# Kernel tuning notes

Measured on AMD Instinct MI355X. Metric: run time of the kernel, lower is better.

Reference implementation:

```python
import jax, jax.numpy as jnp
import numpy as np

NUM_GROUPS = 16
MINIS_PER_GROUP = 16
MINIS_PER_TOK = 4
HIDDEN = 8192
N_TOKENS = 8192


def setup_inputs() -> dict:
    key = jax.random.key(0)
    k1, k2, k3 = jax.random.split(key, 3)
    hidden_states = jax.random.normal(k1, (N_TOKENS, HIDDEN), dtype=jnp.float32)
    # nn.Linear weight: [num_groups, hidden]
    group_gate_w = jax.random.normal(k2, (NUM_GROUPS, HIDDEN), dtype=jnp.float32) * 0.02
    # mini_gates parameter: [num_groups, hidden, minis_per_group]
    mini_gates = jax.random.normal(k3, (NUM_GROUPS, HIDDEN, MINIS_PER_GROUP), dtype=jnp.float32) * 0.02
    return {"hidden_states": hidden_states, "group_gate_w": group_gate_w, "mini_gates": mini_gates}


def reference(hidden_states, group_gate_w, mini_gates):
    # Tier 1: group gate
    group_logits = hidden_states @ group_gate_w.T                      # [N, G]
    group_probs = jax.nn.softmax(group_logits.astype(jnp.float32), axis=-1)
    top_group_probs = jnp.max(group_probs, axis=-1)                    # [N]
    top_group_indices = jnp.argmax(group_probs, axis=-1)               # [N]

    # Tier 2: per-token mini-gate. Instead of gathering a huge [N, H, E]
    # tensor (as the torch code does), compute logits for ALL groups
    # ([N, G, E] is tiny) and select the chosen group's row — same math.
    all_mini_logits = jnp.einsum('nh,ghe->nge', hidden_states, mini_gates)  # [N, G, E]
    mini_logits = jnp.take_along_axis(
        all_mini_logits, top_group_indices[:, None, None], axis=1
    )[:, 0, :]                                                         # [N, E]
    mini_probs = jax.nn.softmax(mini_logits.astype(jnp.float32), axis=-1)

    topk_mini_probs, topk_mini_indices = jax.lax.top_k(mini_probs, MINIS_PER_TOK)
    final_probs = top_group_probs[:, None] * topk_mini_probs
    final_probs = final_probs / jnp.sum(final_probs, axis=-1, keepdims=True)

    global_expert_indices = top_group_indices[:, None] * MINIS_PER_GROUP + topk_mini_indices

    group_aux_loss = jnp.sum(jnp.mean(group_probs, axis=0) ** 2)
    mini_aux_loss = jnp.sum(jnp.mean(mini_probs, axis=0) ** 2)
    total_aux_loss = group_aux_loss + mini_aux_loss

    return (final_probs.astype(hidden_states.dtype), global_expert_indices, total_aux_loss)
```

## Files before the change

kernel.cpp:

```cpp
#include <hip/hip_runtime.h>
#include <math.h>

#define N_TOK 8192
#define HID   8192
#define NG    16
#define NE    16
#define KC    512
#define NCHUNK (HID / KC)
#define TPB   16

#define OFF_CNT   0u
#define OFF_GSUM  64u
#define OFF_ESUM  128u
#define OFF_NTIL  192u
#define ZERO_BYTES 256u
#define OFF_BUCK  256u
#define OFF_SCHED (OFF_BUCK + NG*N_TOK*4)
#define OFF_MGT   (OFF_SCHED + 2048*4)

__device__ __forceinline__ void glds16(const float* gp, float* lp) {
    __builtin_amdgcn_global_load_lds(
        (const __attribute__((address_space(1))) void*)gp,
        (__attribute__((address_space(3))) void*)lp, 16, 0, 0);
}

#define RS_ROUND(o, half)                                                 \
  {                                                                       \
    const bool hi_ = (lane & (o)) != 0;                                   \
    _Pragma("unroll")                                                     \
    for (int i_ = 0; i_ < (half); ++i_) {                                 \
      double s_ = hi_ ? acc64[i_] : acc64[i_ + (half)];                   \
      double r_ = __shfl_xor(s_, (o));                                    \
      acc64[i_] = (hi_ ? acc64[i_ + (half)] : acc64[i_]) + r_;            \
    }                                                                     \
  }

#define DOT8(t, w0, w1)                                                   \
    (aC[2*(t)].x*(w0).x + aC[2*(t)].y*(w0).y + aC[2*(t)].z*(w0).z +       \
     aC[2*(t)].w*(w0).w + aC[2*(t)+1].x*(w1).x + aC[2*(t)+1].y*(w1).y +   \
     aC[2*(t)+1].z*(w1).z + aC[2*(t)+1].w*(w1).w)

__global__ __launch_bounds__(256, 2) void k_group(
    const float* __restrict__ hid, const float* __restrict__ gw,
    int* __restrict__ cnt, int* __restrict__ buckets, float* __restrict__ gsum)
{
    __shared__ float Wl[2][NG * KC];
    const int tid  = threadIdx.x;
    const int lane = tid & 63;
    const int wv   = tid >> 6;
    const int t0   = blockIdx.x * TPB + wv * 4;
    const float* __restrict__ a0 = hid + (size_t)t0 * HID;

    #pragma unroll
    for (int j = 0; j < 8; ++j) {
        int m = wv * 8 + j;
        glds16(gw + (size_t)(m >> 1) * HID + (m & 1) * 256 + 4 * lane,
               &Wl[0][m * 256]);
    }
    float4 areg[8];
    #pragma unroll
    for (int t = 0; t < 4; ++t) {
        areg[2*t]   = *(const float4*)&a0[(size_t)t * HID + 4 * lane];
        areg[2*t+1] = *(const float4*)&a0[(size_t)t * HID + 256 + 4 * lane];
    }

    double acc64[64];
    #pragma unroll
    for (int i = 0; i < 64; ++i) acc64[i] = 0.0;

    for (int c = 0; c < NCHUNK; ++c) {
        __syncthreads();
        float4 aC[8];
        #pragma unroll
        for (int i = 0; i < 8; ++i) aC[i] = areg[i];
        if (c + 1 < NCHUNK) {
            const int kb = (c + 1) * KC;
            #pragma unroll
            for (int j = 0; j < 8; ++j) {
                int m = wv * 8 + j;
                glds16(gw + (size_t)(m >> 1) * HID + kb + (m & 1) * 256 + 4 * lane,
                       &Wl[(c + 1) & 1][m * 256]);
            }
            #pragma unroll
            for (int t = 0; t < 4; ++t) {
                areg[2*t]   = *(const float4*)&a0[(size_t)t * HID + kb + 4 * lane];
                areg[2*t+1] = *(const float4*)&a0[(size_t)t * HID + kb + 256 + 4 * lane];
            }
        }
        const float* Wc = &Wl[c & 1][0];
        #pragma unroll
        for (int g = 0; g < NG; ++g) {
            float4 w0 = *(const float4*)&Wc[g * KC + 4 * lane];
            float4 w1 = *(const float4*)&Wc[g * KC + 256 + 4 * lane];
            #pragma unroll
            for (int t = 0; t < 4; ++t)
                acc64[t * 16 + g] += (double)DOT8(t, w0, w1);
        }
    }

    RS_ROUND(32, 32) RS_ROUND(16, 16) RS_ROUND(8, 8)
    RS_ROUND(4, 4)   RS_ROUND(2, 2)   RS_ROUND(1, 1)
    float v = (float)acc64[0];
    float mx = v;
    #pragma unroll
    for (int o = 8; o; o >>= 1) mx = fmaxf(mx, __shfl_xor(mx, o));
    float p = expf(v - mx);
    float s = p;
    #pragma unroll
    for (int o = 8; o; o >>= 1) s += __shfl_xor(s, o);
    p /= s;
    float x = p;
    x += __shfl_xor(x, 16);
    x += __shfl_xor(x, 32);
    if (lane < 16) unsafeAtomicAdd(&gsum[lane], x);
    int gi = lane & 15; float bv = v;
    #pragma unroll
    for (int o = 8; o; o >>= 1) {
        float ov = __shfl_xor(bv, o);
        int   og = __shfl_xor(gi, o);
        if (ov > bv || (ov == bv && og < gi)) { bv = ov; gi = og; }
    }
    if ((lane & 15) == 0) {
        int t = t0 + (lane >> 4);
        int pos = atomicAdd(&cnt[gi], 1);
        buckets[gi * N_TOK + pos] = t;
    }
}

__global__ __launch_bounds__(256) void k_tr(
    const float* __restrict__ mg, float* __restrict__ mgT)
{
    const int g  = blockIdx.x >> 7;
    const int kb = (blockIdx.x & 127) * 64;
    const int e  = threadIdx.x & 15;
    const int kq = threadIdx.x >> 4;
    const int k0 = kb + 4 * kq;
    const float* src = mg + (size_t)g * HID * NE;
    float4 v;
    v.x = src[(size_t)(k0 + 0) * NE + e];
    v.y = src[(size_t)(k0 + 1) * NE + e];
    v.z = src[(size_t)(k0 + 2) * NE + e];
    v.w = src[(size_t)(k0 + 3) * NE + e];
    *(float4*)&mgT[(size_t)(g * NE + e) * HID + k0] = v;
}

__global__ void k_sched(const int* __restrict__ cnt, int* __restrict__ sched,
                        int* __restrict__ ntile)
{
    __shared__ int pref[NG + 1];
    if (threadIdx.x == 0) {
        int s = 0;
        for (int g = 0; g < NG; ++g) { pref[g] = s; s += (cnt[g] + TPB - 1) / TPB; }
        pref[NG] = s; *ntile = s;
    }
    __syncthreads();
    int total = pref[NG];
    for (int i = threadIdx.x; i < total; i += blockDim.x) {
        int g = 0;
        while (g < NG - 1 && i >= pref[g + 1]) ++g;
        sched[i] = (g << 16) | (i - pref[g]);
    }
}

__global__ __launch_bounds__(256, 2) void k_mini(
    const float* __restrict__ hid, const float* __restrict__ mgT,
    const int* __restrict__ cnt, const int* __restrict__ buckets,
    const int* __restrict__ sched, const int* __restrict__ ntile,
    float* __restrict__ out, float* __restrict__ esum)
{
    if ((int)blockIdx.x >= *ntile) return;
    const int enc  = sched[blockIdx.x];
    const int g    = enc >> 16;
    const int tile = enc & 0xffff;
    const int n    = cnt[g] - tile * TPB;

    __shared__ float Wl[2][NE * KC];
    __shared__ int   rows[TPB];
    __shared__ float sm[256];
    const int tid  = threadIdx.x;
    const int lane = tid & 63;
    const int wv   = tid >> 6;
    const float* __restrict__ wg = mgT + (size_t)g * NE * HID;

    #pragma unroll
    for (int j = 0; j < 8; ++j) {
        int m = wv * 8 + j;
        glds16(wg + (size_t)(m >> 1) * HID + (m & 1) * 256 + 4 * lane,
               &Wl[0][m * 256]);
    }
    if (tid < TPB)
        rows[tid] = buckets[g * N_TOK + tile * TPB + min(tid, n - 1)];
    __syncthreads();
    const float* at[4];
    #pragma unroll
    for (int t = 0; t < 4; ++t) at[t] = hid + (size_t)rows[wv * 4 + t] * HID;

    float4 areg[8];
    #pragma unroll
    for (int t = 0; t < 4; ++t) {
        areg[2*t]   = *(const float4*)&at[t][4 * lane];
        areg[2*t+1] = *(const float4*)&at[t][256 + 4 * lane];
    }
    double acc64[64];
    #pragma unroll
    for (int i = 0; i < 64; ++i) acc64[i] = 0.0;

    for (int c = 0; c < NCHUNK; ++c) {
        __syncthreads();
        float4 aC[8];
        #pragma unroll
        for (int i = 0; i < 8; ++i) aC[i] = areg[i];
        if (c + 1 < NCHUNK) {
            const int kb = (c + 1) * KC;
            #pragma unroll
            for (int j = 0; j < 8; ++j) {
                int m = wv * 8 + j;
                glds16(wg + (size_t)(m >> 1) * HID + kb + (m & 1) * 256 + 4 * lane,
                       &Wl[(c + 1) & 1][m * 256]);
            }
            #pragma unroll
            for (int t = 0; t < 4; ++t) {
                areg[2*t]   = *(const float4*)&at[t][kb + 4 * lane];
                areg[2*t+1] = *(const float4*)&at[t][kb + 256 + 4 * lane];
            }
        }
        const float* Wc = &Wl[c & 1][0];
        #pragma unroll
        for (int e = 0; e < NE; ++e) {
            float4 w0 = *(const float4*)&Wc[e * KC + 4 * lane];
            float4 w1 = *(const float4*)&Wc[e * KC + 256 + 4 * lane];
            #pragma unroll
            for (int t = 0; t < 4; ++t)
                acc64[t * 16 + e] += (double)DOT8(t, w0, w1);
        }
    }

    RS_ROUND(32, 32) RS_ROUND(16, 16) RS_ROUND(8, 8)
    RS_ROUND(4, 4)   RS_ROUND(2, 2)   RS_ROUND(1, 1)
    const int tl = wv * 4 + (lane >> 4);
    float v = (float)acc64[0];
    float mx = v;
    #pragma unroll
    for (int o = 8; o; o >>= 1) mx = fmaxf(mx, __shfl_xor(mx, o));
    float p = expf(v - mx);
    float s = p;
    #pragma unroll
    for (int o = 8; o; o >>= 1) s += __shfl_xor(s, o);
    p /= s;
    float x = (tl < n) ? p : 0.f;
    x += __shfl_xor(x, 16);
    x += __shfl_xor(x, 32);
    if (lane < 16) unsafeAtomicAdd(&esum[lane], x);

    sm[tid] = p;
    __syncthreads();
    if ((tid & 15) == 0) {
        int tt = tid >> 4;
        if (tt < n) {
            float pe[NE];
            #pragma unroll
            for (int e = 0; e < NE; ++e) pe[e] = sm[tt * 16 + e];
            unsigned used = 0;
            float tv[4]; int ti[4];
            #pragma unroll
            for (int j = 0; j < 4; ++j) {
                float best = -1.f; int bi = 0;
                #pragma unroll
                for (int e = 0; e < NE; ++e)
                    if (!((used >> e) & 1u) && pe[e] > best) { best = pe[e]; bi = e; }
                used |= 1u << bi; tv[j] = best; ti[j] = bi;
            }
            float inv4 = 1.f / (tv[0] + tv[1] + tv[2] + tv[3]);
            int t = rows[tt];
            #pragma unroll
            for (int j = 0; j < 4; ++j) {
                out[t * 4 + j]             = tv[j] * inv4;
                out[N_TOK * 4 + t * 4 + j] = (float)(g * NE + ti[j]);
            }
        }
    }
}

__global__ void k_aux(const float* __restrict__ gsum, const float* __restrict__ esum,
                      float* __restrict__ out)
{
    if (threadIdx.x == 0) {
        float a = 0.f;
        for (int g = 0; g < NG; ++g) { float m = gsum[g] * (1.f / N_TOK); a += m * m; }
        for (int e = 0; e < NE; ++e) { float m = esum[e] * (1.f / N_TOK); a += m * m; }
        out[N_TOK * 8] = a;
    }
}

extern "C" void kernel_launch(void* const* d_in, const int* in_sizes, int n_in,
                              void* d_out, int out_size, void* d_ws, size_t ws_size,
                              hipStream_t stream) {
    const float* hid = (const float*)d_in[0];
    const float* gw  = (const float*)d_in[1];
    const float* mg  = (const float*)d_in[2];
    float* out = (float*)d_out;
    char*  ws  = (char*)d_ws;
    int*    cnt     = (int*)   (ws + OFF_CNT);
    float*  gsum    = (float*) (ws + OFF_GSUM);
    float*  esum    = (float*) (ws + OFF_ESUM);
    int*    ntile   = (int*)   (ws + OFF_NTIL);
    int*    buckets = (int*)   (ws + OFF_BUCK);
    int*    sched   = (int*)   (ws + OFF_SCHED);
    float*  mgT     = (float*) (ws + OFF_MGT);

    hipMemsetAsync(d_ws, 0, ZERO_BYTES, stream);

    k_tr<<<2048, 256, 0, stream>>>(mg, mgT);
    k_group<<<N_TOK / TPB, 256, 0, stream>>>(hid, gw, cnt, buckets, gsum);
    k_sched<<<1, 256, 0, stream>>>(cnt, sched, ntile);
    k_mini<<<N_TOK / TPB + NG, 256, 0, stream>>>(hid, mgT, cnt, buckets, sched, ntile, out, esum);
    k_aux<<<1, 64, 0, stream>>>(gsum, esum, out);
}
```

Baseline: 535.4 us.

## Switch gating dot products to fp32 FMA with 512-thread blocks and smaller chunks

Both gating kernels move from double-precision accumulators (64 doubles per lane) to 32 fp32 accumulators using fused multiply-adds. Blocks grow to 512 threads with 2 tokens per wave, and the K chunk shrinks to 256. The first reduction step becomes a plain xor-32 shuffle, and the epilogue indexing is adjusted to match. The goal is to cut register pressure and the slow fp64 converts and adds so occupancy rises and the kernels become bandwidth-bound. The cost is lower accumulation precision, which could flip argmax or top-k ties against the reference.

```diff
diff --git a/kernel.cpp b/kernel.cpp
--- a/kernel.cpp
+++ b/kernel.cpp
@@ -5,9 +5,10 @@
 #define HID   8192
 #define NG    16
 #define NE    16
-#define KC    512
+#define KC    256
 #define NCHUNK (HID / KC)
 #define TPB   16
+#define TPW   2
 
 #define OFF_CNT   0u
 #define OFF_GSUM  64u
@@ -29,18 +30,13 @@
     const bool hi_ = (lane & (o)) != 0;                                   \
     _Pragma("unroll")                                                     \
     for (int i_ = 0; i_ < (half); ++i_) {                                 \
-      double s_ = hi_ ? acc64[i_] : acc64[i_ + (half)];                   \
-      double r_ = __shfl_xor(s_, (o));                                    \
-      acc64[i_] = (hi_ ? acc64[i_ + (half)] : acc64[i_]) + r_;            \
+      float s_ = hi_ ? acc[i_] : acc[i_ + (half)];                        \
+      float r_ = __shfl_xor(s_, (o));                                     \
+      acc[i_] = (hi_ ? acc[i_ + (half)] : acc[i_]) + r_;                  \
     }                                                                     \
   }
 
-#define DOT8(t, w0, w1)                                                   \
-    (aC[2*(t)].x*(w0).x + aC[2*(t)].y*(w0).y + aC[2*(t)].z*(w0).z +       \
-     aC[2*(t)].w*(w0).w + aC[2*(t)+1].x*(w1).x + aC[2*(t)+1].y*(w1).y +   \
-     aC[2*(t)+1].z*(w1).z + aC[2*(t)+1].w*(w1).w)
-
-__global__ __launch_bounds__(256, 2) void k_group(
+__global__ __launch_bounds__(512, 4) void k_group(
     const float* __restrict__ hid, const float* __restrict__ gw,
     int* __restrict__ cnt, int* __restrict__ buckets, float* __restrict__ gsum)
 {
@@ -48,59 +44,57 @@
     const int tid  = threadIdx.x;
     const int lane = tid & 63;
     const int wv   = tid >> 6;
-    const int t0   = blockIdx.x * TPB + wv * 4;
+    const int t0   = blockIdx.x * TPB + wv * TPW;
     const float* __restrict__ a0 = hid + (size_t)t0 * HID;
 
     #pragma unroll
-    for (int j = 0; j < 8; ++j) {
-        int m = wv * 8 + j;
-        glds16(gw + (size_t)(m >> 1) * HID + (m & 1) * 256 + 4 * lane,
-               &Wl[0][m * 256]);
-    }
-    float4 areg[8];
-    #pragma unroll
-    for (int t = 0; t < 4; ++t) {
-        areg[2*t]   = *(const float4*)&a0[(size_t)t * HID + 4 * lane];
-        areg[2*t+1] = *(const float4*)&a0[(size_t)t * HID + 256 + 4 * lane];
-    }
-
-    double acc64[64];
-    #pragma unroll
-    for (int i = 0; i < 64; ++i) acc64[i] = 0.0;
+    for (int j = 0; j < 2; ++j) {
+        int g = wv * 2 + j;
+        glds16(gw + (size_t)g * HID + 4 * lane, &Wl[0][g * KC]);
+    }
+    float4 areg[TPW];
+    #pragma unroll
+    for (int t = 0; t < TPW; ++t)
+        areg[t] = *(const float4*)&a0[(size_t)t * HID + 4 * lane];
+
+    float acc[32];
+    #pragma unroll
+    for (int i = 0; i < 32; ++i) acc[i] = 0.f;
 
     for (int c = 0; c < NCHUNK; ++c) {
         __syncthreads();
-        float4 aC[8];
+        float4 aC[TPW];
         #pragma unroll
-        for (int i = 0; i < 8; ++i) aC[i] = areg[i];
+        for (int t = 0; t < TPW; ++t) aC[t] = areg[t];
         if (c + 1 < NCHUNK) {
             const int kb = (c + 1) * KC;
             #pragma unroll
-            for (int j = 0; j < 8; ++j) {
-                int m = wv * 8 + j;
-                glds16(gw + (size_t)(m >> 1) * HID + kb + (m & 1) * 256 + 4 * lane,
-                       &Wl[(c + 1) & 1][m * 256]);
-            }
-            #pragma unroll
-            for (int t = 0; t < 4; ++t) {
-                areg[2*t]   = *(const float4*)&a0[(size_t)t * HID + kb + 4 * lane];
-                areg[2*t+1] = *(const float4*)&a0[(size_t)t * HID + kb + 256 + 4 * lane];
-            }
+            for (int j = 0; j < 2; ++j) {
+                int g = wv * 2 + j;
+                glds16(gw + (size_t)g * HID + kb + 4 * lane, &Wl[(c + 1) & 1][g * KC]);
+            }
+            #pragma unroll
+            for (int t = 0; t < TPW; ++t)
+                areg[t] = *(const float4*)&a0[(size_t)t * HID + kb + 4 * lane];
         }
         const float* Wc = &Wl[c & 1][0];
         #pragma unroll
         for (int g = 0; g < NG; ++g) {
-            float4 w0 = *(const float4*)&Wc[g * KC + 4 * lane];
-            float4 w1 = *(const float4*)&Wc[g * KC + 256 + 4 * lane];
-            #pragma unroll
-            for (int t = 0; t < 4; ++t)
-                acc64[t * 16 + g] += (double)DOT8(t, w0, w1);
-        }
-    }
-
-    RS_ROUND(32, 32) RS_ROUND(16, 16) RS_ROUND(8, 8)
-    RS_ROUND(4, 4)   RS_ROUND(2, 2)   RS_ROUND(1, 1)
-    float v = (float)acc64[0];
+            float4 w = *(const float4*)&Wc[g * KC + 4 * lane];
+            #pragma unroll
+            for (int t = 0; t < TPW; ++t) {
+                acc[t*16+g] = fmaf(aC[t].x, w.x, acc[t*16+g]);
+                acc[t*16+g] = fmaf(aC[t].y, w.y, acc[t*16+g]);
+                acc[t*16+g] = fmaf(aC[t].z, w.z, acc[t*16+g]);
+                acc[t*16+g] = fmaf(aC[t].w, w.w, acc[t*16+g]);
+            }
+        }
+    }
+
+    #pragma unroll
+    for (int i = 0; i < 32; ++i) acc[i] += __shfl_xor(acc[i], 32);
+    RS_ROUND(16, 16) RS_ROUND(8, 8) RS_ROUND(4, 4) RS_ROUND(2, 2) RS_ROUND(1, 1)
+    float v = acc[0];
     float mx = v;
     #pragma unroll
     for (int o = 8; o; o >>= 1) mx = fmaxf(mx, __shfl_xor(mx, o));
@@ -111,7 +105,6 @@
     p /= s;
     float x = p;
     x += __shfl_xor(x, 16);
-    x += __shfl_xor(x, 32);
     if (lane < 16) unsafeAtomicAdd(&gsum[lane], x);
     int gi = lane & 15; float bv = v;
     #pragma unroll
@@ -120,7 +113,7 @@
         int   og = __shfl_xor(gi, o);
         if (ov > bv || (ov == bv && og < gi)) { bv = ov; gi = og; }
     }
-    if ((lane & 15) == 0) {
+    if (lane < 32 && (lane & 15) == 0) {
         int t = t0 + (lane >> 4);
         int pos = atomicAdd(&cnt[gi], 1);
         buckets[gi * N_TOK + pos] = t;
@@ -162,7 +155,7 @@
     }
 }
 
-__global__ __launch_bounds__(256, 2) void k_mini(
+__global__ __launch_bounds__(512, 4) void k_mini(
     const float* __restrict__ hid, const float* __restrict__ mgT,
     const int* __restrict__ cnt, const int* __restrict__ buckets,
     const int* __restrict__ sched, const int* __restrict__ ntile,
@@ -183,62 +176,61 @@
     const float* __restrict__ wg = mgT + (size_t)g * NE * HID;
 
     #pragma unroll
-    for (int j = 0; j < 8; ++j) {
-        int m = wv * 8 + j;
-        glds16(wg + (size_t)(m >> 1) * HID + (m & 1) * 256 + 4 * lane,
-               &Wl[0][m * 256]);
+    for (int j = 0; j < 2; ++j) {
+        int e = wv * 2 + j;
+        glds16(wg + (size_t)e * HID + 4 * lane, &Wl[0][e * KC]);
     }
     if (tid < TPB)
         rows[tid] = buckets[g * N_TOK + tile * TPB + min(tid, n - 1)];
     __syncthreads();
-    const float* at[4];
-    #pragma unroll
-    for (int t = 0; t < 4; ++t) at[t] = hid + (size_t)rows[wv * 4 + t] * HID;
-
-    float4 areg[8];
-    #pragma unroll
-    for (int t = 0; t < 4; ++t) {
-        areg[2*t]   = *(const float4*)&at[t][4 * lane];
-        areg[2*t+1] = *(const float4*)&at[t][256 + 4 * lane];
-    }
-    double acc64[64];
-    #pragma unroll
-    for (int i = 0; i < 64; ++i) acc64[i] = 0.0;
+    const float* at[TPW];
+    #pragma unroll
+    for (int t = 0; t < TPW; ++t) at[t] = hid + (size_t)rows[wv * TPW + t] * HID;
+
+    float4 areg[TPW];
+    #pragma unroll
+    for (int t = 0; t < TPW; ++t)
+        areg[t] = *(const float4*)&at[t][4 * lane];
+
+    float acc[32];
+    #pragma unroll
+    for (int i = 0; i < 32; ++i) acc[i] = 0.f;
 
     for (int c = 0; c < NCHUNK; ++c) {
         __syncthreads();
-        float4 aC[8];
+        float4 aC[TPW];
         #pragma unroll
-        for (int i = 0; i < 8; ++i) aC[i] = areg[i];
+        for (int t = 0; t < TPW; ++t) aC[t] = areg[t];
         if (c + 1 < NCHUNK) {
             const int kb = (c + 1) * KC;
             #pragma unroll
-            for (int j = 0; j < 8; ++j) {
-                int m = wv * 8 + j;
-                glds16(wg + (size_t)(m >> 1) * HID + kb + (m & 1) * 256 + 4 * lane,
-                       &Wl[(c + 1) & 1][m * 256]);
-            }
-            #pragma unroll
-            for (int t = 0; t < 4; ++t) {
-                areg[2*t]   = *(const float4*)&at[t][kb + 4 * lane];
-                areg[2*t+1] = *(const float4*)&at[t][kb + 256 + 4 * lane];
-            }
+            for (int j = 0; j < 2; ++j) {
+                int e = wv * 2 + j;
+                glds16(wg + (size_t)e * HID + kb + 4 * lane, &Wl[(c + 1) & 1][e * KC]);
+            }
+            #pragma unroll
+            for (int t = 0; t < TPW; ++t)
+                areg[t] = *(const float4*)&at[t][kb + 4 * lane];
         }
         const float* Wc = &Wl[c & 1][0];
         #pragma unroll
         for (int e = 0; e < NE; ++e) {
-            float4 w0 = *(const float4*)&Wc[e * KC + 4 * lane];
-            float4 w1 = *(const float4*)&Wc[e * KC + 256 + 4 * lane];
-            #pragma unroll
-            for (int t = 0; t < 4; ++t)
-                acc64[t * 16 + e] += (double)DOT8(t, w0, w1);
-        }
-    }
-
-    RS_ROUND(32, 32) RS_ROUND(16, 16) RS_ROUND(8, 8)
-    RS_ROUND(4, 4)   RS_ROUND(2, 2)   RS_ROUND(1, 1)
-    const int tl = wv * 4 + (lane >> 4);
-    float v = (float)acc64[0];
+            float4 w = *(const float4*)&Wc[e * KC + 4 * lane];
+            #pragma unroll
+            for (int t = 0; t < TPW; ++t) {
+                acc[t*16+e] = fmaf(aC[t].x, w.x, acc[t*16+e]);
+                acc[t*16+e] = fmaf(aC[t].y, w.y, acc[t*16+e]);
+                acc[t*16+e] = fmaf(aC[t].z, w.z, acc[t*16+e]);
+                acc[t*16+e] = fmaf(aC[t].w, w.w, acc[t*16+e]);
+            }
+        }
+    }
+
+    #pragma unroll
+    for (int i = 0; i < 32; ++i) acc[i] += __shfl_xor(acc[i], 32);
+    RS_ROUND(16, 16) RS_ROUND(8, 8) RS_ROUND(4, 4) RS_ROUND(2, 2) RS_ROUND(1, 1)
+    const int tl = wv * TPW + ((lane >> 4) & 1);
+    float v = acc[0];
     float mx = v;
     #pragma unroll
     for (int o = 8; o; o >>= 1) mx = fmaxf(mx, __shfl_xor(mx, o));
@@ -249,12 +241,11 @@
     p /= s;
     float x = (tl < n) ? p : 0.f;
     x += __shfl_xor(x, 16);
-    x += __shfl_xor(x, 32);
     if (lane < 16) unsafeAtomicAdd(&esum[lane], x);
 
-    sm[tid] = p;
+    if (lane < 32) sm[tl * 16 + (lane & 15)] = p;
     __syncthreads();
-    if ((tid & 15) == 0) {
+    if (tid < 256 && (tid & 15) == 0) {
         int tt = tid >> 4;
         if (tt < n) {
             float pe[NE];
@@ -311,8 +302,8 @@
     hipMemsetAsync(d_ws, 0, ZERO_BYTES, stream);
 
     k_tr<<<2048, 256, 0, stream>>>(mg, mgT);
-    k_group<<<N_TOK / TPB, 256, 0, stream>>>(hid, gw, cnt, buckets, gsum);
+    k_group<<<N_TOK / TPB, 512, 0, stream>>>(hid, gw, cnt, buckets, gsum);
     k_sched<<<1, 256, 0, stream>>>(cnt, sched, ntile);
-    k_mini<<<N_TOK / TPB + NG, 256, 0, stream>>>(hid, mgT, cnt, buckets, sched, ntile, out, esum);
+    k_mini<<<N_TOK / TPB + NG, 512, 0, stream>>>(hid, mgT, cnt, buckets, sched, ntile, out, esum);
     k_aux<<<1, 64, 0, stream>>>(gsum, esum, out);
 }
```

Result: slower. 568.2 us (+6.1%).

## Split hidden dimension across blocks with fp32 partials and separate finalize kernels

Applied to the files above, without the earlier changes.

Both GEMV-style kernels now split the hidden dimension into 8 slices, each block loading its whole weight slice into LDS once and handling 32 tokens. Each block writes per-slice partial logits to workspace, and new finalize kernels sum the slices and do softmax, argmax, bucketing, top-k and aux sums. The double-precision accumulation is replaced with fp32 FMA, which removes costly FP64 work but may change argmax ties and rounding. The change adds more launches and partial-buffer traffic in exchange for more parallelism and no chunk loop.

```diff
diff --git a/kernel.cpp b/kernel.cpp
--- a/kernel.cpp
+++ b/kernel.cpp
@@ -5,9 +5,9 @@
 #define HID   8192
 #define NG    16
 #define NE    16
-#define KC    512
-#define NCHUNK (HID / KC)
-#define TPB   16
+#define NSL   8
+#define KSL   (HID / NSL)
+#define TKB   32
 
 #define OFF_CNT   0u
 #define OFF_GSUM  64u
@@ -16,7 +16,9 @@
 #define ZERO_BYTES 256u
 #define OFF_BUCK  256u
 #define OFF_SCHED (OFF_BUCK + NG*N_TOK*4)
-#define OFF_MGT   (OFF_SCHED + 2048*4)
+#define OFF_GIDX  (OFF_SCHED + 2048*4)
+#define OFF_MGT   (OFF_GIDX + N_TOK*4)
+#define OFF_PART  (OFF_MGT + 16777216u)
 
 __device__ __forceinline__ void glds16(const float* gp, float* lp) {
     __builtin_amdgcn_global_load_lds(
@@ -29,102 +31,109 @@
     const bool hi_ = (lane & (o)) != 0;                                   \
     _Pragma("unroll")                                                     \
     for (int i_ = 0; i_ < (half); ++i_) {                                 \
-      double s_ = hi_ ? acc64[i_] : acc64[i_ + (half)];                   \
-      double r_ = __shfl_xor(s_, (o));                                    \
-      acc64[i_] = (hi_ ? acc64[i_ + (half)] : acc64[i_]) + r_;            \
+      float s_ = hi_ ? acc[i_] : acc[i_ + (half)];                        \
+      float r_ = __shfl_xor(s_, (o));                                     \
+      acc[i_] = (hi_ ? acc[i_ + (half)] : acc[i_]) + r_;                  \
     }                                                                     \
   }
 
-#define DOT8(t, w0, w1)                                                   \
-    (aC[2*(t)].x*(w0).x + aC[2*(t)].y*(w0).y + aC[2*(t)].z*(w0).z +       \
-     aC[2*(t)].w*(w0).w + aC[2*(t)+1].x*(w1).x + aC[2*(t)+1].y*(w1).y +   \
-     aC[2*(t)+1].z*(w1).z + aC[2*(t)+1].w*(w1).w)
-
 __global__ __launch_bounds__(256, 2) void k_group(
     const float* __restrict__ hid, const float* __restrict__ gw,
-    int* __restrict__ cnt, int* __restrict__ buckets, float* __restrict__ gsum)
-{
-    __shared__ float Wl[2][NG * KC];
+    float* __restrict__ pg)
+{
+    __shared__ float Wl[NG * KSL];
     const int tid  = threadIdx.x;
     const int lane = tid & 63;
     const int wv   = tid >> 6;
-    const int t0   = blockIdx.x * TPB + wv * 4;
-    const float* __restrict__ a0 = hid + (size_t)t0 * HID;
-
-    #pragma unroll
-    for (int j = 0; j < 8; ++j) {
-        int m = wv * 8 + j;
-        glds16(gw + (size_t)(m >> 1) * HID + (m & 1) * 256 + 4 * lane,
-               &Wl[0][m * 256]);
-    }
-    float4 areg[8];
-    #pragma unroll
-    for (int t = 0; t < 4; ++t) {
-        areg[2*t]   = *(const float4*)&a0[(size_t)t * HID + 4 * lane];
-        areg[2*t+1] = *(const float4*)&a0[(size_t)t * HID + 256 + 4 * lane];
-    }
-
-    double acc64[64];
-    #pragma unroll
-    for (int i = 0; i < 64; ++i) acc64[i] = 0.0;
-
-    for (int c = 0; c < NCHUNK; ++c) {
-        __syncthreads();
-        float4 aC[8];
-        #pragma unroll
-        for (int i = 0; i < 8; ++i) aC[i] = areg[i];
-        if (c + 1 < NCHUNK) {
-            const int kb = (c + 1) * KC;
+    const int s    = blockIdx.x & 7;
+    const int tb0  = (blockIdx.x >> 3) * TKB;
+    const int ks   = s * KSL;
+
+    #pragma unroll
+    for (int j = 0; j < 16; ++j) {
+        int m = wv * 16 + j;
+        glds16(gw + (size_t)(m >> 2) * HID + ks + (m & 3) * 256 + 4 * lane,
+               &Wl[m * 256]);
+    }
+    __syncthreads();
+
+    const int t0w = tb0 + wv * 8;
+    #pragma unroll 1
+    for (int b = 0; b < 2; ++b) {
+        const int tb = t0w + b * 4;
+        float4 a[4][4];
+        #pragma unroll
+        for (int t = 0; t < 4; ++t) {
             #pragma unroll
-            for (int j = 0; j < 8; ++j) {
-                int m = wv * 8 + j;
-                glds16(gw + (size_t)(m >> 1) * HID + kb + (m & 1) * 256 + 4 * lane,
-                       &Wl[(c + 1) & 1][m * 256]);
+            for (int c = 0; c < 4; ++c)
+                a[t][c] = *(const float4*)
+                    &hid[(size_t)(tb + t) * HID + ks + c * 256 + 4 * lane];
+        }
+        float acc[64];
+        #pragma unroll
+        for (int i = 0; i < 64; ++i) acc[i] = 0.f;
+        #pragma unroll
+        for (int c = 0; c < 4; ++c) {
+            #pragma unroll
+            for (int g = 0; g < NG; ++g) {
+                float4 w = *(const float4*)&Wl[(g * 4 + c) * 256 + 4 * lane];
+                #pragma unroll
+                for (int t = 0; t < 4; ++t) {
+                    acc[t*16+g] = fmaf(a[t][c].x, w.x, acc[t*16+g]);
+                    acc[t*16+g] = fmaf(a[t][c].y, w.y, acc[t*16+g]);
+                    acc[t*16+g] = fmaf(a[t][c].z, w.z, acc[t*16+g]);
+                    acc[t*16+g] = fmaf(a[t][c].w, w.w, acc[t*16+g]);
+                }
             }
-            #pragma unroll
-            for (int t = 0; t < 4; ++t) {
-                areg[2*t]   = *(const float4*)&a0[(size_t)t * HID + kb + 4 * lane];
-                areg[2*t+1] = *(const float4*)&a0[(size_t)t * HID + kb + 256 + 4 * lane];
-            }
-        }
-        const float* Wc = &Wl[c & 1][0];
-        #pragma unroll
-        for (int g = 0; g < NG; ++g) {
-            float4 w0 = *(const float4*)&Wc[g * KC + 4 * lane];
-            float4 w1 = *(const float4*)&Wc[g * KC + 256 + 4 * lane];
-            #pragma unroll
-            for (int t = 0; t < 4; ++t)
-                acc64[t * 16 + g] += (double)DOT8(t, w0, w1);
-        }
-    }
-
-    RS_ROUND(32, 32) RS_ROUND(16, 16) RS_ROUND(8, 8)
-    RS_ROUND(4, 4)   RS_ROUND(2, 2)   RS_ROUND(1, 1)
-    float v = (float)acc64[0];
-    float mx = v;
-    #pragma unroll
-    for (int o = 8; o; o >>= 1) mx = fmaxf(mx, __shfl_xor(mx, o));
-    float p = expf(v - mx);
-    float s = p;
-    #pragma unroll
-    for (int o = 8; o; o >>= 1) s += __shfl_xor(s, o);
-    p /= s;
-    float x = p;
-    x += __shfl_xor(x, 16);
-    x += __shfl_xor(x, 32);
-    if (lane < 16) unsafeAtomicAdd(&gsum[lane], x);
-    int gi = lane & 15; float bv = v;
-    #pragma unroll
-    for (int o = 8; o; o >>= 1) {
-        float ov = __shfl_xor(bv, o);
-        int   og = __shfl_xor(gi, o);
-        if (ov > bv || (ov == bv && og < gi)) { bv = ov; gi = og; }
-    }
-    if ((lane & 15) == 0) {
-        int t = t0 + (lane >> 4);
-        int pos = atomicAdd(&cnt[gi], 1);
-        buckets[gi * N_TOK + pos] = t;
-    }
+        }
+        RS_ROUND(32, 32) RS_ROUND(16, 16) RS_ROUND(8, 8)
+        RS_ROUND(4, 4)   RS_ROUND(2, 2)   RS_ROUND(1, 1)
+        pg[((size_t)s * N_TOK + tb + (lane >> 4)) * 16 + (lane & 15)] = acc[0];
+    }
+}
+
+__global__ __launch_bounds__(256) void k_gfin(
+    const float* __restrict__ pg, int* __restrict__ cnt, int* __restrict__ buckets,
+    float* __restrict__ gsum, int* __restrict__ gidx)
+{
+    const int t    = blockIdx.x * 256 + threadIdx.x;
+    const int lane = threadIdx.x & 63;
+    float l[16];
+    #pragma unroll
+    for (int q = 0; q < 4; ++q) {
+        float4 v = *(const float4*)&pg[(size_t)t * 16 + 4 * q];
+        l[4*q+0] = v.x; l[4*q+1] = v.y; l[4*q+2] = v.z; l[4*q+3] = v.w;
+    }
+    #pragma unroll
+    for (int s2 = 1; s2 < NSL; ++s2) {
+        #pragma unroll
+        for (int q = 0; q < 4; ++q) {
+            float4 v = *(const float4*)&pg[((size_t)s2 * N_TOK + t) * 16 + 4 * q];
+            l[4*q+0] += v.x; l[4*q+1] += v.y; l[4*q+2] += v.z; l[4*q+3] += v.w;
+        }
+    }
+    float mx = l[0];
+    #pragma unroll
+    for (int g = 1; g < NG; ++g) mx = fmaxf(mx, l[g]);
+    float p[16], sum = 0.f;
+    #pragma unroll
+    for (int g = 0; g < NG; ++g) { p[g] = expf(l[g] - mx); sum += p[g]; }
+    float inv = 1.f / sum;
+    #pragma unroll
+    for (int g = 0; g < NG; ++g) p[g] *= inv;
+    #pragma unroll
+    for (int g = 0; g < NG; ++g) {
+        float v = p[g];
+        #pragma unroll
+        for (int o = 32; o; o >>= 1) v += __shfl_xor(v, o);
+        if (lane == 0) unsafeAtomicAdd(&gsum[g], v);
+    }
+    int gi = 0; float bv = l[0];
+    #pragma unroll
+    for (int g = 1; g < NG; ++g) if (l[g] > bv) { bv = l[g]; gi = g; }
+    gidx[t] = gi;
+    int pos = atomicAdd(&cnt[gi], 1);
+    buckets[gi * N_TOK + pos] = t;
 }
 
 __global__ __launch_bounds__(256) void k_tr(
@@ -150,7 +159,7 @@
     __shared__ int pref[NG + 1];
     if (threadIdx.x == 0) {
         int s = 0;
-        for (int g = 0; g < NG; ++g) { pref[g] = s; s += (cnt[g] + TPB - 1) / TPB; }
+        for (int g = 0; g < NG; ++g) { pref[g] = s; s += (cnt[g] + TKB - 1) / TKB; }
         pref[NG] = s; *ntile = s;
     }
     __syncthreads();
@@ -166,118 +175,122 @@
     const float* __restrict__ hid, const float* __restrict__ mgT,
     const int* __restrict__ cnt, const int* __restrict__ buckets,
     const int* __restrict__ sched, const int* __restrict__ ntile,
-    float* __restrict__ out, float* __restrict__ esum)
-{
-    if ((int)blockIdx.x >= *ntile) return;
-    const int enc  = sched[blockIdx.x];
+    float* __restrict__ pm)
+{
+    const int widx = blockIdx.x >> 3;
+    if (widx >= *ntile) return;
+    const int s    = blockIdx.x & 7;
+    const int enc  = sched[widx];
     const int g    = enc >> 16;
     const int tile = enc & 0xffff;
-    const int n    = cnt[g] - tile * TPB;
-
-    __shared__ float Wl[2][NE * KC];
-    __shared__ int   rows[TPB];
-    __shared__ float sm[256];
+    const int n    = cnt[g] - tile * TKB;
+
+    __shared__ float Wl[NE * KSL];
+    __shared__ int   rows[TKB];
     const int tid  = threadIdx.x;
     const int lane = tid & 63;
     const int wv   = tid >> 6;
+    const int ks   = s * KSL;
     const float* __restrict__ wg = mgT + (size_t)g * NE * HID;
 
     #pragma unroll
-    for (int j = 0; j < 8; ++j) {
-        int m = wv * 8 + j;
-        glds16(wg + (size_t)(m >> 1) * HID + (m & 1) * 256 + 4 * lane,
-               &Wl[0][m * 256]);
-    }
-    if (tid < TPB)
-        rows[tid] = buckets[g * N_TOK + tile * TPB + min(tid, n - 1)];
+    for (int j = 0; j < 16; ++j) {
+        int m = wv * 16 + j;
+        glds16(wg + (size_t)(m >> 2) * HID + ks + (m & 3) * 256 + 4 * lane,
+               &Wl[m * 256]);
+    }
+    if (tid < TKB) {
+        int idx = tid < n ? tid : (n - 1);
+        rows[tid] = buckets[g * N_TOK + tile * TKB + idx];
+    }
     __syncthreads();
-    const float* at[4];
-    #pragma unroll
-    for (int t = 0; t < 4; ++t) at[t] = hid + (size_t)rows[wv * 4 + t] * HID;
-
-    float4 areg[8];
-    #pragma unroll
-    for (int t = 0; t < 4; ++t) {
-        areg[2*t]   = *(const float4*)&at[t][4 * lane];
-        areg[2*t+1] = *(const float4*)&at[t][256 + 4 * lane];
-    }
-    double acc64[64];
-    #pragma unroll
-    for (int i = 0; i < 64; ++i) acc64[i] = 0.0;
-
-    for (int c = 0; c < NCHUNK; ++c) {
-        __syncthreads();
-        float4 aC[8];
-        #pragma unroll
-        for (int i = 0; i < 8; ++i) aC[i] = areg[i];
-        if (c + 1 < NCHUNK) {
-            const int kb = (c + 1) * KC;
+
+    #pragma unroll 1
+    for (int b = 0; b < 2; ++b) {
+        const int rbase = wv * 8 + b * 4;
+        float4 a[4][4];
+        #pragma unroll
+        for (int t = 0; t < 4; ++t) {
+            const float* at = hid + (size_t)rows[rbase + t] * HID + ks;
             #pragma unroll
-            for (int j = 0; j < 8; ++j) {
-                int m = wv * 8 + j;
-                glds16(wg + (size_t)(m >> 1) * HID + kb + (m & 1) * 256 + 4 * lane,
-                       &Wl[(c + 1) & 1][m * 256]);
+            for (int c = 0; c < 4; ++c)
+                a[t][c] = *(const float4*)&at[c * 256 + 4 * lane];
+        }
+        float acc[64];
+        #pragma unroll
+        for (int i = 0; i < 64; ++i) acc[i] = 0.f;
+        #pragma unroll
+        for (int c = 0; c < 4; ++c) {
+            #pragma unroll
+            for (int e = 0; e < NE; ++e) {
+                float4 w = *(const float4*)&Wl[(e * 4 + c) * 256 + 4 * lane];
+                #pragma unroll
+                for (int t = 0; t < 4; ++t) {
+                    acc[t*16+e] = fmaf(a[t][c].x, w.x, acc[t*16+e]);
+                    acc[t*16+e] = fmaf(a[t][c].y, w.y, acc[t*16+e]);
+                    acc[t*16+e] = fmaf(a[t][c].z, w.z, acc[t*16+e]);
+                    acc[t*16+e] = fmaf(a[t][c].w, w.w, acc[t*16+e]);
+                }
             }
-            #pragma unroll
-            for (int t = 0; t < 4; ++t) {
-                areg[2*t]   = *(const float4*)&at[t][kb + 4 * lane];
-                areg[2*t+1] = *(const float4*)&at[t][kb + 256 + 4 * lane];
-            }
-        }
-        const float* Wc = &Wl[c & 1][0];
-        #pragma unroll
-        for (int e = 0; e < NE; ++e) {
-            float4 w0 = *(const float4*)&Wc[e * KC + 4 * lane];
-            float4 w1 = *(const float4*)&Wc[e * KC + 256 + 4 * lane];
-            #pragma unroll
-            for (int t = 0; t < 4; ++t)
-                acc64[t * 16 + e] += (double)DOT8(t, w0, w1);
-        }
-    }
-
-    RS_ROUND(32, 32) RS_ROUND(16, 16) RS_ROUND(8, 8)
-    RS_ROUND(4, 4)   RS_ROUND(2, 2)   RS_ROUND(1, 1)
-    const int tl = wv * 4 + (lane >> 4);
-    float v = (float)acc64[0];
-    float mx = v;
-    #pragma unroll
-    for (int o = 8; o; o >>= 1) mx = fmaxf(mx, __shfl_xor(mx, o));
-    float p = expf(v - mx);
-    float s = p;
-    #pragma unroll
-    for (int o = 8; o; o >>= 1) s += __shfl_xor(s, o);
-    p /= s;
-    float x = (tl < n) ? p : 0.f;
-    x += __shfl_xor(x, 16);
-    x += __shfl_xor(x, 32);
-    if (lane < 16) unsafeAtomicAdd(&esum[lane], x);
-
-    sm[tid] = p;
-    __syncthreads();
-    if ((tid & 15) == 0) {
-        int tt = tid >> 4;
-        if (tt < n) {
-            float pe[NE];
-            #pragma unroll
-            for (int e = 0; e < NE; ++e) pe[e] = sm[tt * 16 + e];
-            unsigned used = 0;
-            float tv[4]; int ti[4];
-            #pragma unroll
-            for (int j = 0; j < 4; ++j) {
-                float best = -1.f; int bi = 0;
-                #pragma unroll
-                for (int e = 0; e < NE; ++e)
-                    if (!((used >> e) & 1u) && pe[e] > best) { best = pe[e]; bi = e; }
-                used |= 1u << bi; tv[j] = best; ti[j] = bi;
-            }
-            float inv4 = 1.f / (tv[0] + tv[1] + tv[2] + tv[3]);
-            int t = rows[tt];
-            #pragma unroll
-            for (int j = 0; j < 4; ++j) {
-                out[t * 4 + j]             = tv[j] * inv4;
-                out[N_TOK * 4 + t * 4 + j] = (float)(g * NE + ti[j]);
-            }
-        }
+        }
+        RS_ROUND(32, 32) RS_ROUND(16, 16) RS_ROUND(8, 8)
+        RS_ROUND(4, 4)   RS_ROUND(2, 2)   RS_ROUND(1, 1)
+        pm[((size_t)s * N_TOK + rows[rbase + (lane >> 4)]) * 16 + (lane & 15)] = acc[0];
+    }
+}
+
+__global__ __launch_bounds__(256) void k_mfin(
+    const float* __restrict__ pm, const int* __restrict__ gidx,
+    float* __restrict__ out, float* __restrict__ esum)
+{
+    const int t    = blockIdx.x * 256 + threadIdx.x;
+    const int lane = threadIdx.x & 63;
+    float l[16];
+    #pragma unroll
+    for (int q = 0; q < 4; ++q) {
+        float4 v = *(const float4*)&pm[(size_t)t * 16 + 4 * q];
+        l[4*q+0] = v.x; l[4*q+1] = v.y; l[4*q+2] = v.z; l[4*q+3] = v.w;
+    }
+    #pragma unroll
+    for (int s2 = 1; s2 < NSL; ++s2) {
+        #pragma unroll
+        for (int q = 0; q < 4; ++q) {
+            float4 v = *(const float4*)&pm[((size_t)s2 * N_TOK + t) * 16 + 4 * q];
+            l[4*q+0] += v.x; l[4*q+1] += v.y; l[4*q+2] += v.z; l[4*q+3] += v.w;
+        }
+    }
+    float mx = l[0];
+    #pragma unroll
+    for (int e = 1; e < NE; ++e) mx = fmaxf(mx, l[e]);
+    float p[16], sum = 0.f;
+    #pragma unroll
+    for (int e = 0; e < NE; ++e) { p[e] = expf(l[e] - mx); sum += p[e]; }
+    float inv = 1.f / sum;
+    #pragma unroll
+    for (int e = 0; e < NE; ++e) p[e] *= inv;
+    #pragma unroll
+    for (int e = 0; e < NE; ++e) {
+        float v = p[e];
+        #pragma unroll
+        for (int o = 32; o; o >>= 1) v += __shfl_xor(v, o);
+        if (lane == 0) unsafeAtomicAdd(&esum[e], v);
+    }
+    const int g = gidx[t];
+    unsigned used = 0;
+    float tv[4]; int ti[4];
+    #pragma unroll
+    for (int j = 0; j < 4; ++j) {
+        float best = -1.f; int bi = 0;
+        #pragma unroll
+        for (int e = 0; e < NE; ++e)
+            if (!((used >> e) & 1u) && p[e] > best) { best = p[e]; bi = e; }
+        used |= 1u << bi; tv[j] = best; ti[j] = bi;
+    }
+    float inv4 = 1.f / (tv[0] + tv[1] + tv[2] + tv[3]);
+    #pragma unroll
+    for (int j = 0; j < 4; ++j) {
+        out[t * 4 + j]             = tv[j] * inv4;
+        out[N_TOK * 4 + t * 4 + j] = (float)(g * NE + ti[j]);
     }
 }
 
@@ -306,13 +319,18 @@
     int*    ntile   = (int*)   (ws + OFF_NTIL);
     int*    buckets = (int*)   (ws + OFF_BUCK);
     int*    sched   = (int*)   (ws + OFF_SCHED);
+    int*    gidx    = (int*)   (ws + OFF_GIDX);
     float*  mgT     = (float*) (ws + OFF_MGT);
+    float*  part    = (float*) (ws + OFF_PART);
 
     hipMemsetAsync(d_ws, 0, ZERO_BYTES, stream);
 
-    k_tr<<<2048, 256, 0, stream>>>(mg, mgT);
-    k_group<<<N_TOK / TPB, 256, 0, stream>>>(hid, gw, cnt, buckets, gsum);
+    k_tr   <<<2048, 256, 0, stream>>>(mg, mgT);
+    k_group<<<(N_TOK / TKB) * NSL, 256, 0, stream>>>(hid, gw, part);
+    k_gfin <<<N_TOK / 256, 256, 0, stream>>>(part, cnt, buckets, gsum, gidx);
     k_sched<<<1, 256, 0, stream>>>(cnt, sched, ntile);
-    k_mini<<<N_TOK / TPB + NG, 256, 0, stream>>>(hid, mgT, cnt, buckets, sched, ntile, out, esum);
-    k_aux<<<1, 64, 0, stream>>>(gsum, esum, out);
-}
+    k_mini <<<(N_TOK / TKB + NG) * NSL, 256, 0, stream>>>(hid, mgT, cnt, buckets,
+                                                          sched, ntile, part);
+    k_mfin <<<N_TOK / 256, 256, 0, stream>>>(part, gidx, out, esum);
+    k_aux  <<<1, 64, 0, stream>>>(gsum, esum, out);
+}
```

Result: slower. 917.7 us (+71.4%).
